# Kernel tuning notes

Measured on AMD Instinct MI355X. Metric: run time of the kernel, lower is better.

Reference implementation:

```python
import jax, jax.numpy as jnp
import numpy as np

T, K, H, I, E = 8192, 2, 1024, 2816, 8


def setup_inputs() -> dict:
    key = jax.random.key(0)
    k1, k2, k3, k4, k5 = jax.random.split(key, 5)
    hidden_states = jax.random.normal(k1, (T, H), dtype=jnp.float32)
    expert_routing_table = jax.random.randint(k2, (T, K), 0, E)
    router_weights = jax.random.uniform(k3, (T, K), dtype=jnp.float32)
    # permuted_weights=True: weights stored so forward is x @ w
    # w13: fused gate+up proj [E, H, 2I]; w2: down proj [E, I, H]
    w13 = jax.random.normal(k4, (E, H, 2 * I), dtype=jnp.float32) * (1.0 / np.sqrt(H))
    w2 = jax.random.normal(k5, (E, I, H), dtype=jnp.float32) * (1.0 / np.sqrt(I))
    return {
        "hidden_states": hidden_states,
        "expert_routing_table": expert_routing_table,
        "router_weights": router_weights,
        "w13": w13,
        "w2": w2,
    }


def reference(hidden_states, expert_routing_table, router_weights, w13, w2):
    # Semantics of hpu.mixture_of_experts with activation='silu':
    # out[t] = sum_k rw[t,k] * ( (silu(x@w1g[e]) * (x@w1u[e])) @ w2[e] ), e = table[t,k]
    n_experts = w13.shape[0]
    inter = w2.shape[1]
    # per-token combine coefficient for each expert: [T, E]
    onehot = jax.nn.one_hot(expert_routing_table, n_experts, dtype=hidden_states.dtype)  # [T,K,E]
    coeff = jnp.einsum("tke,tk->te", onehot, router_weights)
    out = jnp.zeros_like(hidden_states)
    for e in range(n_experts):
        gu = hidden_states @ w13[e]            # [T, 2I]
        gate, up = gu[:, :inter], gu[:, inter:]
        h = jax.nn.silu(gate) * up             # [T, I]
        out = out + coeff[:, e:e + 1] * (h @ w2[e])
    return out
```

## Files before the change

### kernel.cpp

```cpp
#include <hip/hip_runtime.h>

typedef unsigned short u16;
typedef unsigned int u32;
typedef __bf16 bf16x8 __attribute__((ext_vector_type(8)));
typedef float f32x4 __attribute__((ext_vector_type(4)));
typedef u16 u16x4 __attribute__((ext_vector_type(4)));

#define T_TOK 8192
#define HDIM 1024
#define IDIM 2816
#define NEXP 8
#define NPAIR (T_TOK * 2)
#define MAXRB 71

#define XB_OFF   (131072u)
#define W13T_OFF (XB_OFF + 16777216u)
#define W2T_OFF  (W13T_OFF + 92274688u)
#define H_OFF    (W2T_OFF + 46137344u)
#define WS_NEED  ((size_t)H_OFF + 102367232u)

__device__ __forceinline__ u16 f2bf(float f) {
  u32 u = __builtin_bit_cast(u32, f);
  u32 r = u + 0x7fffu + ((u >> 16) & 1u);
  return (u16)(r >> 16);
}

#define GLD16(g, l) __builtin_amdgcn_global_load_lds( \
    (const __attribute__((address_space(1))) void*)(g), \
    (__attribute__((address_space(3))) void*)(l), 16, 0, 0)

#define WAITVM(N) asm volatile("s_waitcnt vmcnt(" #N ")" ::: "memory")

__device__ __forceinline__ void pbar() {
  __builtin_amdgcn_sched_barrier(0);
  asm volatile("" ::: "memory");
  __builtin_amdgcn_s_barrier();
  asm volatile("" ::: "memory");
  __builtin_amdgcn_sched_barrier(0);
}

__global__ void init_meta(int* meta) {
  if (threadIdx.x < 16) meta[threadIdx.x] = 0;
}

__global__ void count_k(const int* __restrict__ routing, int* __restrict__ meta) {
  int i = blockIdx.x * 256 + threadIdx.x;
  if (i < NPAIR) atomicAdd(&meta[routing[i]], 1);
}

__global__ void scan_fill(int* __restrict__ meta, int* __restrict__ pairs) {
  if (threadIdx.x == 0) {
    int rb = 0;
    for (int e = 0; e < NEXP; ++e) {
      meta[16 + e] = rb * 256;
      int nrb = (meta[e] + 255) >> 8;
      for (int i = 0; i < nrb; ++i) meta[32 + rb + i] = e;
      rb += nrb;
    }
    meta[24] = rb;
  }
  for (int i = threadIdx.x; i < MAXRB * 256; i += 256) pairs[i] = -1;
}

__global__ void scatter_k(const int* __restrict__ routing, int* __restrict__ meta,
                          int* __restrict__ pairs) {
  int i = blockIdx.x * 256 + threadIdx.x;
  if (i < NPAIR) {
    int e = routing[i];
    int pos = atomicAdd(&meta[8 + e], 1);
    pairs[meta[16 + e] + pos] = i;
  }
}

__global__ void conv_x(const float* __restrict__ in, u16* __restrict__ out) {
  int i = blockIdx.x * 256 + threadIdx.x;
  float4 v = ((const float4*)in)[i];
  u16x4 o = { f2bf(v.x), f2bf(v.y), f2bf(v.z), f2bf(v.w) };
  ((u16x4*)out)[i] = o;
}

__global__ void transpose_cvt(const float* __restrict__ in, u16* __restrict__ out,
                              int R, int C) {
  __shared__ float tile[64][65];
  size_t base = (size_t)blockIdx.z * (size_t)R * (size_t)C;
  in += base; out += base;
  int t = threadIdx.x, tc = t & 63, tr = t >> 6;
  int r0 = blockIdx.y * 64, c0 = blockIdx.x * 64;
#pragma unroll
  for (int p = 0; p < 16; ++p) {
    int r = p * 4 + tr;
    tile[r][tc] = in[(size_t)(r0 + r) * C + c0 + tc];
  }
  __syncthreads();
#pragma unroll
  for (int p = 0; p < 16; ++p) {
    int oc = p * 4 + tr;
    out[(size_t)(c0 + oc) * R + r0 + tc] = f2bf(tile[tc][oc]);
  }
}

__global__ __launch_bounds__(512, 2) void gemm1_k(
    const u16* __restrict__ Xb, const u16* __restrict__ W13T,
    const int* __restrict__ pairs, const int* __restrict__ meta,
    const float* __restrict__ rwf, u16* __restrict__ Hb) {
  int lin = blockIdx.x + 22 * blockIdx.y;
  int xcd = lin & 7, slot = lin >> 3;
  int flat = (xcd < 2) ? xcd * 196 + slot : 392 + (xcd - 2) * 195 + slot;
  int bx = flat / 71, rb = flat % 71;
  if (rb >= meta[24]) return;
  const int e = meta[32 + rb];
  const int bn0 = bx * 128;
  const int tid = threadIdx.x, lane = tid & 63, w = tid >> 6;
  const int wr = w >> 1, wc = w & 1;
  const int rowBase = rb * 256;

  __shared__ __align__(16) u16 lds[65536];
  char* const lb = (char*)lds;

  const int sr = tid >> 3;
  const int swk = ((tid & 7) << 4) ^ ((sr & 7) << 4);
  const u16* aS[4];
#pragma unroll
  for (int h = 0; h < 2; ++h)
#pragma unroll
    for (int j = 0; j < 2; ++j) {
      int pr = pairs[rowBase + h * 128 + j * 64 + sr];
      int tok = pr < 0 ? 0 : (pr >> 1);
      aS[h * 2 + j] = Xb + (size_t)tok * HDIM + (swk >> 1);
    }
  const u16* wBase = W13T + (size_t)e * (2 * IDIM) * HDIM;
  const u16* gS[2]; const u16* uS[2];
#pragma unroll
  for (int j = 0; j < 2; ++j) {
    int r = j * 64 + sr;
    gS[j] = wBase + (size_t)(bn0 + r) * HDIM + (swk >> 1);
    uS[j] = wBase + (size_t)(IDIM + bn0 + r) * HDIM + (swk >> 1);
  }

#define STG_A(b, h, kt) { GLD16(aS[(h)*2+0] + (kt)*64, lb + (b)*32768 + (h)*16384 + tid*16); \
                          GLD16(aS[(h)*2+1] + (kt)*64, lb + (b)*32768 + (h)*16384 + 8192 + tid*16); }
#define STG_G(b, kt)    { GLD16(gS[0] + (kt)*64, lb + 65536 + (b)*16384 + tid*16); \
                          GLD16(gS[1] + (kt)*64, lb + 65536 + (b)*16384 + 8192 + tid*16); }
#define STG_U(b, kt)    { GLD16(uS[0] + (kt)*64, lb + 98304 + (b)*16384 + tid*16); \
                          GLD16(uS[1] + (kt)*64, lb + 98304 + (b)*16384 + 8192 + tid*16); }

  const int l15 = lane & 15, l4 = lane >> 4, l7 = lane & 7;
  const int ko0 = (l4 * 16) ^ (l7 << 4);
  const int ko1 = (64 + l4 * 16) ^ (l7 << 4);
  const int aFB = (wr >> 1) * 16384 + ((wr & 1) * 64 + l15) * 128;
  const int bFB = (wc * 64 + l15) * 128;

#define LDAF(d, b, mf, ko) d = *(const bf16x8*)(lb + (b)*32768 + aFB + (mf)*2048 + (ko))
#define LDGF(d, b, nf, ko) d = *(const bf16x8*)(lb + 65536 + (b)*16384 + bFB + (nf)*2048 + (ko))
#define LDUF(d, b, nf, ko) d = *(const bf16x8*)(lb + 98304 + (b)*16384 + bFB + (nf)*2048 + (ko))

#define MF16(ACC, A, B) \
  _Pragma("unroll") for (int mf = 0; mf < 4; ++mf) \
  _Pragma("unroll") for (int nf = 0; nf < 4; ++nf) \
    ACC[mf][nf] = __builtin_amdgcn_mfma_f32_16x16x32_bf16(A[mf], B[nf], ACC[mf][nf], 0, 0, 0);

  f32x4 accG[4][4], accU[4][4];
  const f32x4 fz = {0.f, 0.f, 0.f, 0.f};
#pragma unroll
  for (int i = 0; i < 4; ++i)
#pragma unroll
    for (int j = 0; j < 4; ++j) { accG[i][j] = fz; accU[i][j] = fz; }

  STG_A(0, 0, 0); STG_A(0, 1, 0); STG_G(0, 0); STG_U(0, 0); STG_A(1, 0, 1);
  WAITVM(4);
  pbar();

  bf16x8 a0[4], a1[4], g0[4], g1[4], u0[4], u1[4];
  for (int i = 0; i < 8; ++i) {
    const int t1 = 2 * i + 1;
    const int n2 = (2 * i + 2) & 15, n3 = (2 * i + 3) & 15;
#pragma unroll
    for (int f = 0; f < 4; ++f) { LDAF(a0[f], 0, f, ko0); LDGF(g0[f], 0, f, ko0); }
    STG_A(1, 1, t1);
    pbar();
    __builtin_amdgcn_s_setprio(1); MF16(accG, a0, g0); __builtin_amdgcn_s_setprio(0);
    WAITVM(4);
    pbar();
#pragma unroll
    for (int f = 0; f < 4; ++f) { LDUF(u0[f], 0, f, ko0); LDAF(a1[f], 0, f, ko1); }
    STG_G(1, t1);
    pbar();
    __builtin_amdgcn_s_setprio(1); MF16(accU, a0, u0); __builtin_amdgcn_s_setprio(0);
    pbar();
#pragma unroll
    for (int f = 0; f < 4; ++f) { LDGF(g1[f], 0, f, ko1); LDUF(u1[f], 0, f, ko1); }
    STG_U(1, t1);
    pbar();
    __builtin_amdgcn_s_setprio(1); MF16(accG, a1, g1); __builtin_amdgcn_s_setprio(0);
    pbar();
    STG_A(0, 0, n2);
    pbar();
    __builtin_amdgcn_s_setprio(1); MF16(accU, a1, u1); __builtin_amdgcn_s_setprio(0);
    WAITVM(4);
    pbar();
#pragma unroll
    for (int f = 0; f < 4; ++f) { LDAF(a0[f], 1, f, ko0); LDGF(g0[f], 1, f, ko0); }
    STG_A(0, 1, n2);
    pbar();
    __builtin_amdgcn_s_setprio(1); MF16(accG, a0, g0); __builtin_amdgcn_s_setprio(0);
    WAITVM(4);
    pbar();
#pragma unroll
    for (int f = 0; f < 4; ++f) { LDUF(u0[f], 1, f, ko0); LDAF(a1[f], 1, f, ko1); }
    STG_G(0, n2);
    pbar();
    __builtin_amdgcn_s_setprio(1); MF16(accU, a0, u0); __builtin_amdgcn_s_setprio(0);
    pbar();
#pragma unroll
    for (int f = 0; f < 4; ++f) { LDGF(g1[f], 1, f, ko1); LDUF(u1[f], 1, f, ko1); }
    STG_U(0, n2);
    pbar();
    __builtin_amdgcn_s_setprio(1); MF16(accG, a1, g1); __builtin_amdgcn_s_setprio(0);
    pbar();
    STG_A(1, 0, n3);
    pbar();
    __builtin_amdgcn_s_setprio(1); MF16(accU, a1, u1); __builtin_amdgcn_s_setprio(0);
    WAITVM(4);
    pbar();
  }
#undef STG_A
#undef STG_G
#undef STG_U
#undef LDAF
#undef LDGF
#undef LDUF

  const int ct = l4;
#pragma unroll
  for (int mf = 0; mf < 4; ++mf) {
#pragma unroll
    for (int j = 0; j < 4; ++j) {
      int m = wr * 64 + mf * 16 + ct * 4 + j;
      int pr = rowBase + m;
      int pair = pairs[pr];
      float rw = pair >= 0 ? rwf[pair] : 0.f;
      u16* hrow = Hb + (size_t)pr * IDIM + bn0 + wc * 64 + l15;
#pragma unroll
      for (int nf = 0; nf < 4; ++nf) {
        float g = accG[mf][nf][j], u = accU[mf][nf][j];
        float s = g / (1.f + __expf(-g));
        hrow[nf * 16] = f2bf(s * u * rw);
      }
    }
  }
}

__global__ __launch_bounds__(512, 2) void gemm2_k(
    const u16* __restrict__ Hb, const u16* __restrict__ W2T,
    const int* __restrict__ pairs, const int* __restrict__ meta,
    float* __restrict__ out) {
  int lin = blockIdx.x + 4 * blockIdx.y + 284 * blockIdx.z;
  int xcd = lin & 7, slot = lin >> 3;
  int flat = xcd * 71 + slot;
  int zz = flat / 284, rm = flat % 284;
  int bx = rm / 71, rb = rm % 71;
  if (rb >= meta[24]) return;
  const int e = meta[32 + rb];
  const int bn0 = bx * 256;
  const int kz = zz * 1408;
  const int tid = threadIdx.x, lane = tid & 63, w = tid >> 6;
  const int wr = w >> 2, wc = w & 3;
  const int rowBase = rb * 256;

  __shared__ __align__(16) u16 lds[65536];
  char* const lb = (char*)lds;

  const int sr = tid >> 3;
  const int swk = ((tid & 7) << 4) ^ ((sr & 7) << 4);
  const u16* aS[4]; const u16* bS[4];
#pragma unroll
  for (int h = 0; h < 2; ++h)
#pragma unroll
    for (int j = 0; j < 2; ++j) {
      int r = h * 128 + j * 64 + sr;
      aS[h * 2 + j] = Hb + (size_t)(rowBase + r) * IDIM + kz + (swk >> 1);
      bS[h * 2 + j] = W2T + (size_t)e * HDIM * IDIM + (size_t)(bn0 + r) * IDIM + kz + (swk >> 1);
    }

#define STG_A2(b, h, kt) { GLD16(aS[(h)*2+0] + (kt)*64, lb + (b)*32768 + (h)*16384 + tid*16); \
                           GLD16(aS[(h)*2+1] + (kt)*64, lb + (b)*32768 + (h)*16384 + 8192 + tid*16); }
#define STG_B2(b, h, kt) { GLD16(bS[(h)*2+0] + (kt)*64, lb + 65536 + (b)*32768 + (h)*16384 + tid*16); \
                           GLD16(bS[(h)*2+1] + (kt)*64, lb + 65536 + (b)*32768 + (h)*16384 + 8192 + tid*16); }

  const int l15 = lane & 15, l4 = lane >> 4, l7 = lane & 7;
  const int ko0 = (l4 * 16) ^ (l7 << 4);
  const int ko1 = (64 + l4 * 16) ^ (l7 << 4);
  const int aFB = wr * 16384 + l15 * 128;
  const int bFB = (wc >> 1) * 16384 + ((wc & 1) * 64 + l15) * 128;

#define LDAF2(d, b, mf, ko) d = *(const bf16x8*)(lb + (b)*32768 + aFB + (mf)*2048 + (ko))
#define LDBF2(d, b, nf, ko) d = *(const bf16x8*)(lb + 65536 + (b)*32768 + bFB + (nf)*2048 + (ko))

#define MF2(AV, BV, NB) \
  _Pragma("unroll") for (int mf = 0; mf < 8; ++mf) \
  _Pragma("unroll") for (int nn = 0; nn < 2; ++nn) \
    acc[mf][(NB)+nn] = __builtin_amdgcn_mfma_f32_16x16x32_bf16(AV[mf], BV[(NB)+nn], acc[mf][(NB)+nn], 0, 0, 0);

  f32x4 acc[8][4];
  const f32x4 fz = {0.f, 0.f, 0.f, 0.f};
#pragma unroll
  for (int i = 0; i < 8; ++i)
#pragma unroll
    for (int j = 0; j < 4; ++j) acc[i][j] = fz;

  STG_A2(0, 0, 0); STG_A2(0, 1, 0); STG_B2(0, 0, 0); STG_B2(0, 1, 0); STG_A2(1, 0, 1);
  WAITVM(2);
  pbar();

  bf16x8 aK0[8], aK1[8], bK0[4], bK1[4];
  for (int i = 0; i < 11; ++i) {
    const int t1 = 2 * i + 1;
    const int n2 = (2 * i + 2 < 22) ? 2 * i + 2 : 0;
    const int n3 = (2 * i + 3 < 22) ? 2 * i + 3 : 0;
#pragma unroll
    for (int f = 0; f < 8; ++f) LDAF2(aK0[f], 0, f, ko0);
#pragma unroll
    for (int f = 0; f < 4; ++f) LDBF2(bK0[f], 0, f, ko0);
    STG_A2(1, 1, t1);
    pbar();
    __builtin_amdgcn_s_setprio(1); MF2(aK0, bK0, 0); __builtin_amdgcn_s_setprio(0);
    pbar();
#pragma unroll
    for (int f = 0; f < 8; ++f) LDAF2(aK1[f], 0, f, ko1);
    STG_B2(1, 0, t1);
    pbar();
    __builtin_amdgcn_s_setprio(1); MF2(aK0, bK0, 2); __builtin_amdgcn_s_setprio(0);
    pbar();
#pragma unroll
    for (int f = 0; f < 4; ++f) LDBF2(bK1[f], 0, f, ko1);
    STG_B2(1, 1, t1);
    pbar();
    __builtin_amdgcn_s_setprio(1); MF2(aK1, bK1, 0); __builtin_amdgcn_s_setprio(0);
    pbar();
    STG_A2(0, 0, n2);
    pbar();
    __builtin_amdgcn_s_setprio(1); MF2(aK1, bK1, 2); __builtin_amdgcn_s_setprio(0);
    WAITVM(2);
    pbar();
#pragma unroll
    for (int f = 0; f < 8; ++f) LDAF2(aK0[f], 1, f, ko0);
#pragma unroll
    for (int f = 0; f < 4; ++f) LDBF2(bK0[f], 1, f, ko0);
    STG_A2(0, 1, n2);
    pbar();
    __builtin_amdgcn_s_setprio(1); MF2(aK0, bK0, 0); __builtin_amdgcn_s_setprio(0);
    pbar();
#pragma unroll
    for (int f = 0; f < 8; ++f) LDAF2(aK1[f], 1, f, ko1);
    STG_B2(0, 0, n2);
    pbar();
    __builtin_amdgcn_s_setprio(1); MF2(aK0, bK0, 2); __builtin_amdgcn_s_setprio(0);
    pbar();
#pragma unroll
    for (int f = 0; f < 4; ++f) LDBF2(bK1[f], 1, f, ko1);
    STG_B2(0, 1, n2);
    pbar();
    __builtin_amdgcn_s_setprio(1); MF2(aK1, bK1, 0); __builtin_amdgcn_s_setprio(0);
    pbar();
    STG_A2(1, 0, n3);
    pbar();
    __builtin_amdgcn_s_setprio(1); MF2(aK1, bK1, 2); __builtin_amdgcn_s_setprio(0);
    WAITVM(2);
    pbar();
  }
#undef STG_A2
#undef STG_B2
#undef LDAF2
#undef LDBF2

  const int ct = l4;
#pragma unroll
  for (int mf = 0; mf < 8; ++mf) {
#pragma unroll
    for (int j = 0; j < 4; ++j) {
      int m = wr * 128 + mf * 16 + ct * 4 + j;
      int pair = pairs[rowBase + m];
      if (pair >= 0) {
        float* orow = out + (size_t)(pair >> 1) * HDIM + bn0 + wc * 64 + l15;
#pragma unroll
        for (int nf = 0; nf < 4; ++nf) atomicAdd(orow + nf * 16, acc[mf][nf][j]);
      }
    }
  }
}

extern "C" void kernel_launch(void* const* d_in, const int* in_sizes, int n_in,
                              void* d_out, int out_size, void* d_ws, size_t ws_size,
                              hipStream_t stream) {
  const float* X = (const float*)d_in[0];
  const int* routing = (const int*)d_in[1];
  const float* rwf = (const float*)d_in[2];
  const float* w13 = (const float*)d_in[3];
  const float* w2 = (const float*)d_in[4];
  float* out = (float*)d_out;
  char* ws = (char*)d_ws;

  hipMemsetAsync(d_out, 0, (size_t)T_TOK * HDIM * sizeof(float), stream);
  if (ws_size < WS_NEED) return;

  int* meta = (int*)ws;
  int* pairs = (int*)(ws + 1024);
  u16* Xb = (u16*)(ws + XB_OFF);
  u16* W13T = (u16*)(ws + W13T_OFF);
  u16* W2T = (u16*)(ws + W2T_OFF);
  u16* Hb = (u16*)(ws + H_OFF);

  init_meta<<<1, 64, 0, stream>>>(meta);
  count_k<<<NPAIR / 256, 256, 0, stream>>>(routing, meta);
  scan_fill<<<1, 256, 0, stream>>>(meta, pairs);
  scatter_k<<<NPAIR / 256, 256, 0, stream>>>(routing, meta, pairs);
  conv_x<<<(T_TOK * HDIM / 4) / 256, 256, 0, stream>>>(X, Xb);
  transpose_cvt<<<dim3(5632 / 64, 1024 / 64, NEXP), 256, 0, stream>>>(w13, W13T, 1024, 5632);
  transpose_cvt<<<dim3(1024 / 64, 2816 / 64, NEXP), 256, 0, stream>>>(w2, W2T, 2816, 1024);
  gemm1_k<<<dim3(22, MAXRB), 512, 0, stream>>>(Xb, W13T, pairs, meta, rwf, Hb);
  gemm2_k<<<dim3(4, MAXRB, 2), 512, 0, stream>>>(Hb, W2T, pairs, meta, out);
}
```

Before: 653.2 us.

## Replace gemm2 atomics with per-row partial buffer and gather-reduce; vectorize conversions

The down-projection kernel no longer splits K or uses float atomics into the output. Each block now computes a full-K 128x128 tile with 256 threads and writes plain stores into a partial buffer indexed by sorted row. A new reduce kernel uses an inverse map from each (token, k) pair to its sorted row and sums the two partial rows per token, which also removes the output memset. The x conversion and weight transpose kernels are vectorized to 8-wide bf16 stores, and pair filling is moved into a separate multi-block kernel. The cost is extra traffic for the partial buffer, which reuses the W13T workspace after gemm1 has finished with it, plus one more kernel launch.

```diff
diff --git a/kernel.cpp b/kernel.cpp
--- a/kernel.cpp
+++ b/kernel.cpp
@@ -5,6 +5,7 @@
 typedef __bf16 bf16x8 __attribute__((ext_vector_type(8)));
 typedef float f32x4 __attribute__((ext_vector_type(4)));
 typedef u16 u16x4 __attribute__((ext_vector_type(4)));
+typedef u16 u16x8 __attribute__((ext_vector_type(8)));
 
 #define T_TOK 8192
 #define HDIM 1024
@@ -13,7 +14,7 @@
 #define NPAIR (T_TOK * 2)
 #define MAXRB 71
 
-#define XB_OFF   (131072u)
+#define XB_OFF   (147456u)
 #define W13T_OFF (XB_OFF + 16777216u)
 #define W2T_OFF  (W13T_OFF + 92274688u)
 #define H_OFF    (W2T_OFF + 46137344u)
@@ -48,7 +49,7 @@
   if (i < NPAIR) atomicAdd(&meta[routing[i]], 1);
 }
 
-__global__ void scan_fill(int* __restrict__ meta, int* __restrict__ pairs) {
+__global__ void scan_k(int* __restrict__ meta) {
   if (threadIdx.x == 0) {
     int rb = 0;
     for (int e = 0; e < NEXP; ++e) {
@@ -59,43 +60,57 @@
     }
     meta[24] = rb;
   }
-  for (int i = threadIdx.x; i < MAXRB * 256; i += 256) pairs[i] = -1;
+}
+
+__global__ void fill_pairs(int* __restrict__ pairs) {
+  pairs[blockIdx.x * 256 + threadIdx.x] = -1;
 }
 
 __global__ void scatter_k(const int* __restrict__ routing, int* __restrict__ meta,
-                          int* __restrict__ pairs) {
+                          int* __restrict__ pairs, int* __restrict__ inv) {
   int i = blockIdx.x * 256 + threadIdx.x;
   if (i < NPAIR) {
     int e = routing[i];
     int pos = atomicAdd(&meta[8 + e], 1);
-    pairs[meta[16 + e] + pos] = i;
+    int row = meta[16 + e] + pos;
+    pairs[row] = i;
+    inv[i] = row;
   }
 }
 
 __global__ void conv_x(const float* __restrict__ in, u16* __restrict__ out) {
   int i = blockIdx.x * 256 + threadIdx.x;
-  float4 v = ((const float4*)in)[i];
-  u16x4 o = { f2bf(v.x), f2bf(v.y), f2bf(v.z), f2bf(v.w) };
-  ((u16x4*)out)[i] = o;
+  float4 a = ((const float4*)in)[2 * i];
+  float4 b = ((const float4*)in)[2 * i + 1];
+  u16x8 o = { f2bf(a.x), f2bf(a.y), f2bf(a.z), f2bf(a.w),
+              f2bf(b.x), f2bf(b.y), f2bf(b.z), f2bf(b.w) };
+  ((u16x8*)out)[i] = o;
 }
 
 __global__ void transpose_cvt(const float* __restrict__ in, u16* __restrict__ out,
                               int R, int C) {
-  __shared__ float tile[64][65];
+  __shared__ float tile[64][68];
   size_t base = (size_t)blockIdx.z * (size_t)R * (size_t)C;
   in += base; out += base;
-  int t = threadIdx.x, tc = t & 63, tr = t >> 6;
+  int t = threadIdx.x;
   int r0 = blockIdx.y * 64, c0 = blockIdx.x * 64;
-#pragma unroll
-  for (int p = 0; p < 16; ++p) {
-    int r = p * 4 + tr;
-    tile[r][tc] = in[(size_t)(r0 + r) * C + c0 + tc];
+  int lr = t >> 4, lc4 = (t & 15) * 4;
+#pragma unroll
+  for (int p = 0; p < 4; ++p) {
+    float4 v = *(const float4*)&in[(size_t)(r0 + p * 16 + lr) * C + c0 + lc4];
+    tile[p * 16 + lr][lc4] = v.x; tile[p * 16 + lr][lc4 + 1] = v.y;
+    tile[p * 16 + lr][lc4 + 2] = v.z; tile[p * 16 + lr][lc4 + 3] = v.w;
   }
   __syncthreads();
-#pragma unroll
-  for (int p = 0; p < 16; ++p) {
-    int oc = p * 4 + tr;
-    out[(size_t)(c0 + oc) * R + r0 + tc] = f2bf(tile[tc][oc]);
+  int oc = t >> 2, g0 = (t & 3) * 2;
+#pragma unroll
+  for (int gg = 0; gg < 2; ++gg) {
+    int g = g0 + gg;
+    u16x8 o = { f2bf(tile[g * 8 + 0][oc]), f2bf(tile[g * 8 + 1][oc]),
+                f2bf(tile[g * 8 + 2][oc]), f2bf(tile[g * 8 + 3][oc]),
+                f2bf(tile[g * 8 + 4][oc]), f2bf(tile[g * 8 + 5][oc]),
+                f2bf(tile[g * 8 + 6][oc]), f2bf(tile[g * 8 + 7][oc]) };
+    *(u16x8*)&out[(size_t)(c0 + oc) * R + r0 + g * 8] = o;
   }
 }
 
@@ -250,122 +265,94 @@
   }
 }
 
-__global__ __launch_bounds__(512, 2) void gemm2_k(
+__global__ __launch_bounds__(256, 2) void gemm2_k(
     const u16* __restrict__ Hb, const u16* __restrict__ W2T,
-    const int* __restrict__ pairs, const int* __restrict__ meta,
-    float* __restrict__ out) {
-  int lin = blockIdx.x + 4 * blockIdx.y + 284 * blockIdx.z;
+    const int* __restrict__ meta, float* __restrict__ part) {
+  int lin = blockIdx.y + 142 * blockIdx.x;
   int xcd = lin & 7, slot = lin >> 3;
-  int flat = xcd * 71 + slot;
-  int zz = flat / 284, rm = flat % 284;
-  int bx = rm / 71, rb = rm % 71;
-  if (rb >= meta[24]) return;
-  const int e = meta[32 + rb];
-  const int bn0 = bx * 256;
-  const int kz = zz * 1408;
+  int flat = xcd * 142 + slot;
+  int bx = flat / 142, rb2 = flat % 142;
+  if (rb2 >= meta[24] * 2) return;
+  const int e = meta[32 + (rb2 >> 1)];
+  const int bn0 = bx * 128;
   const int tid = threadIdx.x, lane = tid & 63, w = tid >> 6;
-  const int wr = w >> 2, wc = w & 3;
-  const int rowBase = rb * 256;
-
-  __shared__ __align__(16) u16 lds[65536];
-  char* const lb = (char*)lds;
+  const int wr = w >> 1, wc = w & 1;
+  const int rowBase = rb2 * 128;
+
+  __shared__ __align__(16) u16 lds2[32768];
+  char* const lb = (char*)lds2;
 
   const int sr = tid >> 3;
   const int swk = ((tid & 7) << 4) ^ ((sr & 7) << 4);
   const u16* aS[4]; const u16* bS[4];
 #pragma unroll
-  for (int h = 0; h < 2; ++h)
-#pragma unroll
-    for (int j = 0; j < 2; ++j) {
-      int r = h * 128 + j * 64 + sr;
-      aS[h * 2 + j] = Hb + (size_t)(rowBase + r) * IDIM + kz + (swk >> 1);
-      bS[h * 2 + j] = W2T + (size_t)e * HDIM * IDIM + (size_t)(bn0 + r) * IDIM + kz + (swk >> 1);
-    }
-
-#define STG_A2(b, h, kt) { GLD16(aS[(h)*2+0] + (kt)*64, lb + (b)*32768 + (h)*16384 + tid*16); \
-                           GLD16(aS[(h)*2+1] + (kt)*64, lb + (b)*32768 + (h)*16384 + 8192 + tid*16); }
-#define STG_B2(b, h, kt) { GLD16(bS[(h)*2+0] + (kt)*64, lb + 65536 + (b)*32768 + (h)*16384 + tid*16); \
-                           GLD16(bS[(h)*2+1] + (kt)*64, lb + 65536 + (b)*32768 + (h)*16384 + 8192 + tid*16); }
+  for (int j = 0; j < 4; ++j) {
+    aS[j] = Hb + (size_t)(rowBase + j * 32 + sr) * IDIM + (swk >> 1);
+    bS[j] = W2T + (size_t)e * HDIM * IDIM + (size_t)(bn0 + j * 32 + sr) * IDIM + (swk >> 1);
+  }
+
+#define STG_A2(b, kt) { GLD16(aS[0] + (kt)*64, lb + (b)*16384 + tid*16); \
+                        GLD16(aS[1] + (kt)*64, lb + (b)*16384 + 4096 + tid*16); \
+                        GLD16(aS[2] + (kt)*64, lb + (b)*16384 + 8192 + tid*16); \
+                        GLD16(aS[3] + (kt)*64, lb + (b)*16384 + 12288 + tid*16); }
+#define STG_B2(b, kt) { GLD16(bS[0] + (kt)*64, lb + 32768 + (b)*16384 + tid*16); \
+                        GLD16(bS[1] + (kt)*64, lb + 32768 + (b)*16384 + 4096 + tid*16); \
+                        GLD16(bS[2] + (kt)*64, lb + 32768 + (b)*16384 + 8192 + tid*16); \
+                        GLD16(bS[3] + (kt)*64, lb + 32768 + (b)*16384 + 12288 + tid*16); }
 
   const int l15 = lane & 15, l4 = lane >> 4, l7 = lane & 7;
   const int ko0 = (l4 * 16) ^ (l7 << 4);
   const int ko1 = (64 + l4 * 16) ^ (l7 << 4);
-  const int aFB = wr * 16384 + l15 * 128;
-  const int bFB = (wc >> 1) * 16384 + ((wc & 1) * 64 + l15) * 128;
-
-#define LDAF2(d, b, mf, ko) d = *(const bf16x8*)(lb + (b)*32768 + aFB + (mf)*2048 + (ko))
-#define LDBF2(d, b, nf, ko) d = *(const bf16x8*)(lb + 65536 + (b)*32768 + bFB + (nf)*2048 + (ko))
-
-#define MF2(AV, BV, NB) \
-  _Pragma("unroll") for (int mf = 0; mf < 8; ++mf) \
-  _Pragma("unroll") for (int nn = 0; nn < 2; ++nn) \
-    acc[mf][(NB)+nn] = __builtin_amdgcn_mfma_f32_16x16x32_bf16(AV[mf], BV[(NB)+nn], acc[mf][(NB)+nn], 0, 0, 0);
-
-  f32x4 acc[8][4];
+  const int aFB = (wr * 64 + l15) * 128;
+  const int bFB = (wc * 64 + l15) * 128;
+
+#define LDAF2(d, b, mf, ko) d = *(const bf16x8*)(lb + (b)*16384 + aFB + (mf)*2048 + (ko))
+#define LDBF2(d, b, nf, ko) d = *(const bf16x8*)(lb + 32768 + (b)*16384 + bFB + (nf)*2048 + (ko))
+
+#define MF16v(A, B) \
+  _Pragma("unroll") for (int mf = 0; mf < 4; ++mf) \
+  _Pragma("unroll") for (int nf = 0; nf < 4; ++nf) \
+    acc[mf][nf] = __builtin_amdgcn_mfma_f32_16x16x32_bf16(A[mf], B[nf], acc[mf][nf], 0, 0, 0);
+
+  f32x4 acc[4][4];
   const f32x4 fz = {0.f, 0.f, 0.f, 0.f};
 #pragma unroll
-  for (int i = 0; i < 8; ++i)
+  for (int i = 0; i < 4; ++i)
 #pragma unroll
     for (int j = 0; j < 4; ++j) acc[i][j] = fz;
 
-  STG_A2(0, 0, 0); STG_A2(0, 1, 0); STG_B2(0, 0, 0); STG_B2(0, 1, 0); STG_A2(1, 0, 1);
-  WAITVM(2);
+  STG_A2(0, 0); STG_B2(0, 0); STG_A2(1, 1);
+  WAITVM(4);
   pbar();
 
-  bf16x8 aK0[8], aK1[8], bK0[4], bK1[4];
-  for (int i = 0; i < 11; ++i) {
+  bf16x8 a0[4], a1[4], b0[4], b1[4];
+  for (int i = 0; i < 22; ++i) {
     const int t1 = 2 * i + 1;
-    const int n2 = (2 * i + 2 < 22) ? 2 * i + 2 : 0;
-    const int n3 = (2 * i + 3 < 22) ? 2 * i + 3 : 0;
-#pragma unroll
-    for (int f = 0; f < 8; ++f) LDAF2(aK0[f], 0, f, ko0);
-#pragma unroll
-    for (int f = 0; f < 4; ++f) LDBF2(bK0[f], 0, f, ko0);
-    STG_A2(1, 1, t1);
-    pbar();
-    __builtin_amdgcn_s_setprio(1); MF2(aK0, bK0, 0); __builtin_amdgcn_s_setprio(0);
-    pbar();
-#pragma unroll
-    for (int f = 0; f < 8; ++f) LDAF2(aK1[f], 0, f, ko1);
-    STG_B2(1, 0, t1);
-    pbar();
-    __builtin_amdgcn_s_setprio(1); MF2(aK0, bK0, 2); __builtin_amdgcn_s_setprio(0);
-    pbar();
-#pragma unroll
-    for (int f = 0; f < 4; ++f) LDBF2(bK1[f], 0, f, ko1);
-    STG_B2(1, 1, t1);
-    pbar();
-    __builtin_amdgcn_s_setprio(1); MF2(aK1, bK1, 0); __builtin_amdgcn_s_setprio(0);
-    pbar();
-    STG_A2(0, 0, n2);
-    pbar();
-    __builtin_amdgcn_s_setprio(1); MF2(aK1, bK1, 2); __builtin_amdgcn_s_setprio(0);
-    WAITVM(2);
-    pbar();
-#pragma unroll
-    for (int f = 0; f < 8; ++f) LDAF2(aK0[f], 1, f, ko0);
-#pragma unroll
-    for (int f = 0; f < 4; ++f) LDBF2(bK0[f], 1, f, ko0);
-    STG_A2(0, 1, n2);
-    pbar();
-    __builtin_amdgcn_s_setprio(1); MF2(aK0, bK0, 0); __builtin_amdgcn_s_setprio(0);
-    pbar();
-#pragma unroll
-    for (int f = 0; f < 8; ++f) LDAF2(aK1[f], 1, f, ko1);
-    STG_B2(0, 0, n2);
-    pbar();
-    __builtin_amdgcn_s_setprio(1); MF2(aK0, bK0, 2); __builtin_amdgcn_s_setprio(0);
-    pbar();
-#pragma unroll
-    for (int f = 0; f < 4; ++f) LDBF2(bK1[f], 1, f, ko1);
-    STG_B2(0, 1, n2);
-    pbar();
-    __builtin_amdgcn_s_setprio(1); MF2(aK1, bK1, 0); __builtin_amdgcn_s_setprio(0);
-    pbar();
-    STG_A2(1, 0, n3);
-    pbar();
-    __builtin_amdgcn_s_setprio(1); MF2(aK1, bK1, 2); __builtin_amdgcn_s_setprio(0);
-    WAITVM(2);
+    const int nt0 = (2 * i + 2 < 44) ? 2 * i + 2 : 0;
+    const int nt1 = (2 * i + 3 < 44) ? 2 * i + 3 : 0;
+#pragma unroll
+    for (int f = 0; f < 4; ++f) { LDAF2(a0[f], 0, f, ko0); LDAF2(a1[f], 0, f, ko1);
+                                  LDBF2(b0[f], 0, f, ko0); LDBF2(b1[f], 0, f, ko1); }
+    STG_B2(1, t1);
+    pbar();
+    __builtin_amdgcn_s_setprio(1); MF16v(a0, b0); __builtin_amdgcn_s_setprio(0);
+    pbar();
+    STG_A2(0, nt0);
+    pbar();
+    __builtin_amdgcn_s_setprio(1); MF16v(a1, b1); __builtin_amdgcn_s_setprio(0);
+    WAITVM(4);
+    pbar();
+#pragma unroll
+    for (int f = 0; f < 4; ++f) { LDAF2(a0[f], 1, f, ko0); LDAF2(a1[f], 1, f, ko1);
+                                  LDBF2(b0[f], 1, f, ko0); LDBF2(b1[f], 1, f, ko1); }
+    STG_B2(0, nt0);
+    pbar();
+    __builtin_amdgcn_s_setprio(1); MF16v(a0, b0); __builtin_amdgcn_s_setprio(0);
+    pbar();
+    STG_A2(1, nt1);
+    pbar();
+    __builtin_amdgcn_s_setprio(1); MF16v(a1, b1); __builtin_amdgcn_s_setprio(0);
+    WAITVM(4);
     pbar();
   }
 #undef STG_A2
@@ -373,20 +360,29 @@
 #undef LDAF2
 #undef LDBF2
 
+  WAITVM(0);
   const int ct = l4;
 #pragma unroll
-  for (int mf = 0; mf < 8; ++mf) {
+  for (int mf = 0; mf < 4; ++mf) {
 #pragma unroll
     for (int j = 0; j < 4; ++j) {
-      int m = wr * 128 + mf * 16 + ct * 4 + j;
-      int pair = pairs[rowBase + m];
-      if (pair >= 0) {
-        float* orow = out + (size_t)(pair >> 1) * HDIM + bn0 + wc * 64 + l15;
-#pragma unroll
-        for (int nf = 0; nf < 4; ++nf) atomicAdd(orow + nf * 16, acc[mf][nf][j]);
-      }
+      int m = rowBase + wr * 64 + mf * 16 + ct * 4 + j;
+      float* prow = part + (size_t)m * HDIM + bn0 + wc * 64 + l15;
+#pragma unroll
+      for (int nf = 0; nf < 4; ++nf) prow[nf * 16] = acc[mf][nf][j];
     }
   }
+}
+
+__global__ void reduce_k(const float* __restrict__ part, const int* __restrict__ inv,
+                         float* __restrict__ out) {
+  int t = blockIdx.x;
+  int c = threadIdx.x * 4;
+  int r0 = inv[2 * t], r1 = inv[2 * t + 1];
+  float4 a = *(const float4*)&part[(size_t)r0 * HDIM + c];
+  float4 b = *(const float4*)&part[(size_t)r1 * HDIM + c];
+  float4 o = { a.x + b.x, a.y + b.y, a.z + b.z, a.w + b.w };
+  *(float4*)&out[(size_t)t * HDIM + c] = o;
 }
 
 extern "C" void kernel_launch(void* const* d_in, const int* in_sizes, int n_in,
@@ -400,23 +396,29 @@
   float* out = (float*)d_out;
   char* ws = (char*)d_ws;
 
-  hipMemsetAsync(d_out, 0, (size_t)T_TOK * HDIM * sizeof(float), stream);
-  if (ws_size < WS_NEED) return;
+  if (ws_size < WS_NEED) {
+    hipMemsetAsync(d_out, 0, (size_t)T_TOK * HDIM * sizeof(float), stream);
+    return;
+  }
 
   int* meta = (int*)ws;
   int* pairs = (int*)(ws + 1024);
+  int* inv = (int*)(ws + 73728);
   u16* Xb = (u16*)(ws + XB_OFF);
   u16* W13T = (u16*)(ws + W13T_OFF);
   u16* W2T = (u16*)(ws + W2T_OFF);
   u16* Hb = (u16*)(ws + H_OFF);
+  float* part = (float*)(ws + W13T_OFF);
 
   init_meta<<<1, 64, 0, stream>>>(meta);
   count_k<<<NPAIR / 256, 256, 0, stream>>>(routing, meta);
-  scan_fill<<<1, 256, 0, stream>>>(meta, pairs);
-  scatter_k<<<NPAIR / 256, 256, 0, stream>>>(routing, meta, pairs);
-  conv_x<<<(T_TOK * HDIM / 4) / 256, 256, 0, stream>>>(X, Xb);
+  scan_k<<<1, 64, 0, stream>>>(meta);
+  fill_pairs<<<MAXRB, 256, 0, stream>>>(pairs);
+  scatter_k<<<NPAIR / 256, 256, 0, stream>>>(routing, meta, pairs, inv);
+  conv_x<<<(T_TOK * HDIM / 8) / 256, 256, 0, stream>>>(X, Xb);
   transpose_cvt<<<dim3(5632 / 64, 1024 / 64, NEXP), 256, 0, stream>>>(w13, W13T, 1024, 5632);
   transpose_cvt<<<dim3(1024 / 64, 2816 / 64, NEXP), 256, 0, stream>>>(w2, W2T, 2816, 1024);
   gemm1_k<<<dim3(22, MAXRB), 512, 0, stream>>>(Xb, W13T, pairs, meta, rwf, Hb);
-  gemm2_k<<<dim3(4, MAXRB, 2), 512, 0, stream>>>(Hb, W2T, pairs, meta, out);
-}
+  gemm2_k<<<dim3(8, 2 * MAXRB), 256, 0, stream>>>(Hb, W2T, meta, part);
+  reduce_k<<<T_TOK, 256, 0, stream>>>(part, inv, out);
+}
```

Result: faster. 574.2 us (-12.1%).
